# Kernel optimization log

Hardware: AMD Instinct MI355X
Metric: run time of the kernel (lower is better)

The kernel has to match this reference:

```python
import jax, jax.numpy as jnp
import numpy as np

B, S, H, E, K = 8, 4096, 1024, 256, 64
NEG = -1e30  # finite stand-in for -inf to keep grads NaN-free


def setup_inputs() -> dict:
    key = jax.random.key(0)
    ks = jax.random.split(key, 8)
    Hq = H // 4
    sc = 0.02
    return {
        "hidden_states": jax.random.normal(ks[0], (B, S, H), dtype=jnp.float32),
        "attention_mask": jnp.ones((B, S), dtype=jnp.int32),
        "block_boundaries": jnp.sort(jax.random.randint(ks[1], (B, K), 0, S), axis=-1),
        "tok_w1": jax.random.normal(ks[2], (H, Hq), dtype=jnp.float32) * sc,
        "tok_b1": jnp.zeros((Hq,), dtype=jnp.float32),
        "tok_w2": jax.random.normal(ks[3], (Hq, 1), dtype=jnp.float32) * sc,
        "tok_b2": jnp.zeros((1,), dtype=jnp.float32),
        "blk_w1": jax.random.normal(ks[4], (H, Hq), dtype=jnp.float32) * sc,
        "blk_b1": jnp.zeros((Hq,), dtype=jnp.float32),
        "blk_w2": jax.random.normal(ks[5], (Hq, 1), dtype=jnp.float32) * sc,
        "blk_b2": jnp.zeros((1,), dtype=jnp.float32),
        "out_w": jax.random.normal(ks[6], (H, E), dtype=jnp.float32) * sc,
        "out_b": jnp.zeros((E,), dtype=jnp.float32),
    }


def _attn_scores(x, w1, b1, w2, b2):
    # Linear -> Tanh -> Linear(.,1), squeeze last dim
    return (jnp.tanh(x @ w1 + b1) @ w2 + b2)[..., 0]


def reference(hidden_states, attention_mask, block_boundaries,
              tok_w1, tok_b1, tok_w2, tok_b2,
              blk_w1, blk_b1, blk_w2, blk_b2,
              out_w, out_b):
    Bz, Sz, Hz = hidden_states.shape
    Kz = block_boundaries.shape[1]
    pos = jnp.arange(Sz)
    # token -> block id: last boundary <= pos (tokens before first boundary get -1)
    block_id = jax.vmap(lambda bnd: jnp.searchsorted(bnd, pos, side='right') - 1)(block_boundaries)  # [B,S]
    member = block_id[:, :, None] == jnp.arange(Kz)[None, None, :]      # [B,S,K]
    valid = (attention_mask == 1) & (block_id >= 0)                     # [B,S]
    m_full = member & valid[:, :, None]                                 # [B,S,K]

    # stage 1: per-block masked softmax over tokens
    tok_scores = _attn_scores(hidden_states, tok_w1, tok_b1, tok_w2, tok_b2)  # [B,S]
    s = jnp.where(m_full, tok_scores[:, :, None], NEG)
    mx = jnp.max(s, axis=1, keepdims=True)                              # [B,1,K]
    e = jnp.where(m_full, jnp.exp(tok_scores[:, :, None] - mx), 0.0)
    denom = jnp.sum(e, axis=1, keepdims=True)                           # [B,1,K]
    w = jnp.where(denom > 0, e / jnp.maximum(denom, 1e-30), 0.0)
    block_embed = jnp.einsum('bsk,bsd->bkd', w, hidden_states)          # [B,K,H]
    block_valid = denom[:, 0, :] > 0                                    # [B,K] (empty blocks dropped)

    # stage 2: softmax over (non-empty) blocks
    blk_scores = _attn_scores(block_embed, blk_w1, blk_b1, blk_w2, blk_b2)    # [B,K]
    blk_scores = jnp.where(block_valid, blk_scores, NEG)
    bw = jax.nn.softmax(blk_scores, axis=-1)
    func = jnp.einsum('bk,bkd->bd', bw, block_embed)                    # [B,H]

    out = func @ out_w + out_b                                          # [B,E]
    return out / jnp.maximum(jnp.linalg.norm(out, axis=-1, keepdims=True), 1e-12)
```

## Files before the change

kernel.cpp:

```cpp
#include <hip/hip_runtime.h>
#include <math.h>
#include <limits.h>

#define BB 8
#define SS 4096
#define HH 1024
#define EE 256
#define KK 64
#define HQ 256
#define NEGF -1e30f

typedef short bf16x8 __attribute__((ext_vector_type(8)));
typedef float f32x4  __attribute__((ext_vector_type(4)));

__device__ inline short f2bf(float x) {
    unsigned u = __float_as_uint(x);
    unsigned r = (u + 0x7fffu + ((u >> 16) & 1u)) >> 16;
    return (short)r;
}

__device__ inline unsigned pk2bf(float lo, float hi) {
    unsigned a = __float_as_uint(lo) + 0x8000u;
    unsigned b = __float_as_uint(hi) + 0x8000u;
    return (a >> 16) | (b & 0xffff0000u);
}

__global__ __launch_bounds__(256) void convert_both_kernel(
    const float* __restrict__ tok_w1, const float* __restrict__ blk_w1,
    short* __restrict__ w1s_tok, short* __restrict__ w1s_blk)
{
    const int kb = blockIdx.x & 31, which = blockIdx.x >> 5;
    const float* src = which ? blk_w1 : tok_w1;
    short* dst = which ? w1s_blk : w1s_tok;
    const int n = threadIdx.x;
    for (int kk = 0; kk < 32; kk++)
        dst[kb * 8192 + n * 32 + kk] = f2bf(src[(kb * 32 + kk) * HQ + n]);
}

__global__ __launch_bounds__(256, 4) void mfma_score4_kernel(
    const float* __restrict__ X, const short* __restrict__ w1s,
    const float* __restrict__ b1, const float* __restrict__ w2,
    const float* __restrict__ b2, float* __restrict__ out)
{
    __shared__ __attribute__((aligned(16))) short As[2][1024];
    __shared__ float part[4][32];

    const int t = threadIdx.x;
    const int wv = t >> 6, lane = t & 63, lo = lane & 15, q = lane >> 4;
    const long row0 = (long)blockIdx.x * 32;

    f32x4 acc[2][4];
#pragma unroll
    for (int i = 0; i < 2; i++)
#pragma unroll
        for (int j = 0; j < 4; j++) acc[i][j] = (f32x4){0.f, 0.f, 0.f, 0.f};

    const int c = t >> 1, half = t & 1;
    const int srow = ((c >> 6) << 4) + (c & 15);
    const int skofs = ((c >> 4) & 3) * 8 + half * 4;
    const float* xs = X + (row0 + srow) * HH + skofs;
    short* const dst0 = &As[0][c * 8 + half * 4];
    short* const dst1 = &As[1][c * 8 + half * 4];
    const short* wp = w1s + (wv * 64 + lo) * 32 + q * 8;

    {
        float4 v = *(const float4*)xs;
        unsigned u0 = pk2bf(v.x, v.y), u1 = pk2bf(v.z, v.w);
        ((unsigned*)dst0)[0] = u0; ((unsigned*)dst0)[1] = u1;
    }
    bf16x8 bA[4], bB[4];
#pragma unroll
    for (int ct = 0; ct < 4; ct++)
        bA[ct] = *(const bf16x8*)(wp + ct * 512);
    __syncthreads();

    for (int kb = 0; kb < 32; kb += 2) {
        {
            float4 v = *(const float4*)(xs + (kb + 1) * 32);
#pragma unroll
            for (int ct = 0; ct < 4; ct++)
                bB[ct] = *(const bf16x8*)(wp + (kb + 1) * 8192 + ct * 512);
            bf16x8 af[2];
#pragma unroll
            for (int rt = 0; rt < 2; rt++)
                af[rt] = *(bf16x8*)(&As[0][(rt * 64 + q * 16 + lo) * 8]);
#pragma unroll
            for (int rt = 0; rt < 2; rt++)
#pragma unroll
                for (int ct = 0; ct < 4; ct++)
                    acc[rt][ct] = __builtin_amdgcn_mfma_f32_16x16x32_bf16(
                        af[rt], bA[ct], acc[rt][ct], 0, 0, 0);
            unsigned u0 = pk2bf(v.x, v.y), u1 = pk2bf(v.z, v.w);
            ((unsigned*)dst1)[0] = u0; ((unsigned*)dst1)[1] = u1;
        }
        __syncthreads();
        {
            const int k2 = (kb + 2 < 32) ? kb + 2 : 31;
            float4 v = *(const float4*)(xs + k2 * 32);
#pragma unroll
            for (int ct = 0; ct < 4; ct++)
                bA[ct] = *(const bf16x8*)(wp + k2 * 8192 + ct * 512);
            bf16x8 af[2];
#pragma unroll
            for (int rt = 0; rt < 2; rt++)
                af[rt] = *(bf16x8*)(&As[1][(rt * 64 + q * 16 + lo) * 8]);
#pragma unroll
            for (int rt = 0; rt < 2; rt++)
#pragma unroll
                for (int ct = 0; ct < 4; ct++)
                    acc[rt][ct] = __builtin_amdgcn_mfma_f32_16x16x32_bf16(
                        af[rt], bB[ct], acc[rt][ct], 0, 0, 0);
            unsigned u0 = pk2bf(v.x, v.y), u1 = pk2bf(v.z, v.w);
            ((unsigned*)dst0)[0] = u0; ((unsigned*)dst0)[1] = u1;
        }
        __syncthreads();
    }

    float rowpart[2][4];
#pragma unroll
    for (int rt = 0; rt < 2; rt++)
#pragma unroll
        for (int r = 0; r < 4; r++) rowpart[rt][r] = 0.f;
#pragma unroll
    for (int ct = 0; ct < 4; ct++) {
        const int cc = wv * 64 + ct * 16 + lo;
        const float b1c = b1[cc], w2c = w2[cc];
#pragma unroll
        for (int rt = 0; rt < 2; rt++)
#pragma unroll
            for (int r = 0; r < 4; r++)
                rowpart[rt][r] += tanhf(acc[rt][ct][r] + b1c) * w2c;
    }
#pragma unroll
    for (int rt = 0; rt < 2; rt++)
#pragma unroll
        for (int r = 0; r < 4; r++) {
            float v = rowpart[rt][r];
            v += __shfl_down(v, 8, 64);
            v += __shfl_down(v, 4, 64);
            v += __shfl_down(v, 2, 64);
            v += __shfl_down(v, 1, 64);
            rowpart[rt][r] = v;
        }
    if (lo == 0)
#pragma unroll
        for (int rt = 0; rt < 2; rt++)
#pragma unroll
            for (int r = 0; r < 4; r++)
                part[wv][rt * 16 + q * 4 + r] = rowpart[rt][r];
    __syncthreads();
    if (t < 32)
        out[row0 + t] = part[0][t] + part[1][t] + part[2][t] + part[3][t] + b2[0];
}

__global__ __launch_bounds__(256) void block_stats_kernel(
    const float* __restrict__ scores, const int* __restrict__ mask,
    const int* __restrict__ bnd, float* __restrict__ bden,
    float* __restrict__ wtok, float* __restrict__ embed)
{
    const int b = blockIdx.x >> 6, k = blockIdx.x & 63;
    const int start = bnd[b * KK + k];
    const int end = (k == KK - 1) ? SS : bnd[b * KK + k + 1];
    const int tid = threadIdx.x;
    __shared__ float r[4];
    __shared__ float mshared, dshared;

    *((float4*)(embed + (long)blockIdx.x * HH) + tid) = (float4){0.f, 0.f, 0.f, 0.f};
    if (k == 0)
        for (int s = tid; s < start; s += 256) wtok[b * SS + s] = 0.f;

    float m = NEGF;
    for (int s = start + tid; s < end; s += 256)
        if (mask[b * SS + s] == 1) m = fmaxf(m, scores[b * SS + s]);
    for (int off = 32; off > 0; off >>= 1) m = fmaxf(m, __shfl_down(m, off, 64));
    if ((tid & 63) == 0) r[tid >> 6] = m;
    __syncthreads();
    if (tid == 0) mshared = fmaxf(fmaxf(r[0], r[1]), fmaxf(r[2], r[3]));
    __syncthreads();
    m = mshared;

    float d = 0.f;
    for (int s = start + tid; s < end; s += 256)
        if (mask[b * SS + s] == 1) d += expf(scores[b * SS + s] - m);
    for (int off = 32; off > 0; off >>= 1) d += __shfl_down(d, off, 64);
    __syncthreads();
    if ((tid & 63) == 0) r[tid >> 6] = d;
    __syncthreads();
    if (tid == 0) {
        float den = r[0] + r[1] + r[2] + r[3];
        bden[blockIdx.x] = den;
        dshared = (den > 0.f) ? 1.f / fmaxf(den, 1e-30f) : 0.f;
    }
    __syncthreads();
    const float inv = dshared;
    for (int s = start + tid; s < end; s += 256)
        wtok[b * SS + s] = (mask[b * SS + s] == 1) ? expf(scores[b * SS + s] - m) * inv : 0.f;
}

#define TCH 16
__global__ __launch_bounds__(256) void block_embed4_kernel(
    const float* __restrict__ hidden, const float* __restrict__ wtok,
    const int* __restrict__ bnd, float* __restrict__ embed)
{
    const int b = blockIdx.x >> 8;
    const int ch = blockIdx.x & 255;
    const int t = threadIdx.x;
    __shared__ int bsh[KK];
    __shared__ float wsh[TCH];
    const int s0 = ch * TCH, s1 = s0 + TCH;
    if (t < KK) bsh[t] = bnd[b * KK + t];
    if (t >= 64 && t < 64 + TCH) wsh[t - 64] = wtok[b * SS + s0 + (t - 64)];
    __syncthreads();

    int cur = -1;
#pragma unroll
    for (int i = 0; i < KK; i++) cur = (bsh[i] <= s0) ? i : cur;
    const int nxt = (cur + 1 < KK) ? bsh[cur + 1] : INT_MAX;

    const float* hr0 = hidden + ((long)b * SS + s0) * HH + t;
    float a0 = 0.f, a1 = 0.f, a2 = 0.f, a3 = 0.f;

    if (nxt >= s1 && cur >= 0) {
#pragma unroll
        for (int i = 0; i < TCH; i++) {
            const float w = wsh[i];
            const float* hr = hr0 + (long)i * HH;
            a0 = fmaf(w, hr[0], a0);
            a1 = fmaf(w, hr[256], a1);
            a2 = fmaf(w, hr[512], a2);
            a3 = fmaf(w, hr[768], a3);
        }
        float* e = embed + ((long)b * KK + cur) * HH;
        atomicAdd(e + t, a0); atomicAdd(e + t + 256, a1);
        atomicAdd(e + t + 512, a2); atomicAdd(e + t + 768, a3);
        return;
    }

    bool any = false;
    for (int s = s0; s < s1; s++) {
        while (cur + 1 < KK && bsh[cur + 1] <= s) {
            if (any) {
                float* e = embed + ((long)b * KK + cur) * HH;
                atomicAdd(e + t, a0); atomicAdd(e + t + 256, a1);
                atomicAdd(e + t + 512, a2); atomicAdd(e + t + 768, a3);
                a0 = a1 = a2 = a3 = 0.f; any = false;
            }
            cur++;
        }
        if (cur < 0) continue;
        const float w = wsh[s - s0];
        const float* hr = hr0 + (long)(s - s0) * HH;
        a0 = fmaf(w, hr[0], a0);
        a1 = fmaf(w, hr[256], a1);
        a2 = fmaf(w, hr[512], a2);
        a3 = fmaf(w, hr[768], a3);
        any = true;
    }
    if (any) {
        float* e = embed + ((long)b * KK + cur) * HH;
        atomicAdd(e + t, a0); atomicAdd(e + t + 256, a1);
        atomicAdd(e + t + 512, a2); atomicAdd(e + t + 768, a3);
    }
}

__global__ __launch_bounds__(256) void finalize_ab_kernel(
    const float* __restrict__ embed, const float* __restrict__ bscores,
    const float* __restrict__ bden, const float* __restrict__ out_w,
    float* __restrict__ osum)
{
    const int b = blockIdx.x >> 3, hc = blockIdx.x & 7;
    const int t = threadIdx.x;
    __shared__ float bw[KK];
    __shared__ float fpart[2][128];
    __shared__ float fsh[128];

    if (t < KK) {
        float s = (bden[b * KK + t] > 0.f) ? bscores[b * KK + t] : NEGF;
        float m = s;
        for (int off = 32; off > 0; off >>= 1) m = fmaxf(m, __shfl_xor(m, off, 64));
        float e = expf(s - m);
        float d = e;
        for (int off = 32; off > 0; off >>= 1) d += __shfl_xor(d, off, 64);
        bw[t] = e / d;
    }
    __syncthreads();

    {
        const int hh = t & 127, kh = t >> 7;
        const float* ep = embed + ((long)b * KK + kh * 32) * HH + hc * 128 + hh;
        float f = 0.f;
#pragma unroll 8
        for (int k2 = 0; k2 < 32; k2++)
            f = fmaf(bw[kh * 32 + k2], ep[(long)k2 * HH], f);
        fpart[kh][hh] = f;
    }
    __syncthreads();
    if (t < 128) fsh[t] = fpart[0][t] + fpart[1][t];
    __syncthreads();

    float acc = 0.f;
    const float* wpp = out_w + (long)(hc * 128) * EE + t;
#pragma unroll 8
    for (int h = 0; h < 128; h++)
        acc = fmaf(fsh[h], wpp[(long)h * EE], acc);
    osum[(long)(b * 8 + hc) * EE + t] = acc;
}

__global__ __launch_bounds__(256) void finalize_c_kernel(
    const float* __restrict__ osum, const float* __restrict__ out_b,
    float* __restrict__ outp)
{
    const int b = blockIdx.x, t = threadIdx.x;
    __shared__ float r4[4];
    float o = out_b[t];
#pragma unroll
    for (int hc = 0; hc < 8; hc++)
        o += osum[(long)(b * 8 + hc) * EE + t];
    float sq = o * o;
    for (int off = 32; off > 0; off >>= 1) sq += __shfl_down(sq, off, 64);
    if ((t & 63) == 0) r4[t >> 6] = sq;
    __syncthreads();
    const float nrm = sqrtf(r4[0] + r4[1] + r4[2] + r4[3]);
    outp[b * EE + t] = o / fmaxf(nrm, 1e-12f);
}

extern "C" void kernel_launch(void* const* d_in, const int* in_sizes, int n_in,
                              void* d_out, int out_size, void* d_ws, size_t ws_size,
                              hipStream_t stream) {
    const float* hidden  = (const float*)d_in[0];
    const int*   mask    = (const int*)  d_in[1];
    const int*   bnd     = (const int*)  d_in[2];
    const float* tok_w1  = (const float*)d_in[3];
    const float* tok_b1  = (const float*)d_in[4];
    const float* tok_w2  = (const float*)d_in[5];
    const float* tok_b2  = (const float*)d_in[6];
    const float* blk_w1  = (const float*)d_in[7];
    const float* blk_b1  = (const float*)d_in[8];
    const float* blk_w2  = (const float*)d_in[9];
    const float* blk_b2  = (const float*)d_in[10];
    const float* out_w   = (const float*)d_in[11];
    const float* out_b   = (const float*)d_in[12];

    float* ws      = (float*)d_ws;
    float* wtok    = ws;
    float* embed   = ws + 32768;
    float* scores  = ws + 557056;
    float* bden    = ws + 589824;
    float* bscores = ws + 590336;
    float* osum    = ws + 590848;
    short* w1s_tok = (short*)(ws + 607232);
    short* w1s_blk = w1s_tok + 262144;

    convert_both_kernel<<<64, 256, 0, stream>>>(tok_w1, blk_w1, w1s_tok, w1s_blk);
    mfma_score4_kernel<<<BB * SS / 32, 256, 0, stream>>>(
        hidden, w1s_tok, tok_b1, tok_w2, tok_b2, scores);
    block_stats_kernel<<<BB * KK, 256, 0, stream>>>(
        scores, mask, bnd, bden, wtok, embed);
    block_embed4_kernel<<<BB * SS / TCH, 256, 0, stream>>>(hidden, wtok, bnd, embed);
    mfma_score4_kernel<<<BB * KK / 32, 256, 0, stream>>>(
        embed, w1s_blk, blk_b1, blk_w2, blk_b2, bscores);
    finalize_ab_kernel<<<BB * 8, 256, 0, stream>>>(
        embed, bscores, bden, out_w, osum);
    finalize_c_kernel<<<BB, 256, 0, stream>>>(osum, out_b, (float*)d_out);
}
```

Before: 300.7 us.

## Stage full 32-row activation tile in padded LDS and drop per-step barriers

Measured after the change: 312.2 us. +3.8%, slower.

```diff
diff --git a/kernel.cpp b/kernel.cpp
--- a/kernel.cpp
+++ b/kernel.cpp
@@ -37,83 +37,75 @@
         dst[kb * 8192 + n * 32 + kk] = f2bf(src[(kb * 32 + kk) * HQ + n]);
 }
 
-__global__ __launch_bounds__(256, 4) void mfma_score4_kernel(
+#define APAD 1032
+__global__ __launch_bounds__(256) void mfma_score5_kernel(
     const float* __restrict__ X, const short* __restrict__ w1s,
     const float* __restrict__ b1, const float* __restrict__ w2,
     const float* __restrict__ b2, float* __restrict__ out)
 {
-    __shared__ __attribute__((aligned(16))) short As[2][1024];
+    __shared__ __attribute__((aligned(16))) short As[32 * APAD];
     __shared__ float part[4][32];
 
     const int t = threadIdx.x;
     const int wv = t >> 6, lane = t & 63, lo = lane & 15, q = lane >> 4;
     const long row0 = (long)blockIdx.x * 32;
 
+    const float* xbase = X + row0 * HH + wv * 256 + lane * 4;
+#pragma unroll 8
+    for (int i = 0; i < 32; i++) {
+        float4 v = *(const float4*)(xbase + (long)i * HH);
+        unsigned u0 = pk2bf(v.x, v.y), u1 = pk2bf(v.z, v.w);
+        uint2* d = (uint2*)(&As[i * APAD + wv * 256 + lane * 4]);
+        *d = (uint2){u0, u1};
+    }
+    __syncthreads();
+
     f32x4 acc[2][4];
 #pragma unroll
     for (int i = 0; i < 2; i++)
 #pragma unroll
         for (int j = 0; j < 4; j++) acc[i][j] = (f32x4){0.f, 0.f, 0.f, 0.f};
 
-    const int c = t >> 1, half = t & 1;
-    const int srow = ((c >> 6) << 4) + (c & 15);
-    const int skofs = ((c >> 4) & 3) * 8 + half * 4;
-    const float* xs = X + (row0 + srow) * HH + skofs;
-    short* const dst0 = &As[0][c * 8 + half * 4];
-    short* const dst1 = &As[1][c * 8 + half * 4];
     const short* wp = w1s + (wv * 64 + lo) * 32 + q * 8;
-
-    {
-        float4 v = *(const float4*)xs;
-        unsigned u0 = pk2bf(v.x, v.y), u1 = pk2bf(v.z, v.w);
-        ((unsigned*)dst0)[0] = u0; ((unsigned*)dst0)[1] = u1;
-    }
+    const int aofs = lo * APAD + q * 8;
+
     bf16x8 bA[4], bB[4];
 #pragma unroll
     for (int ct = 0; ct < 4; ct++)
         bA[ct] = *(const bf16x8*)(wp + ct * 512);
-    __syncthreads();
 
     for (int kb = 0; kb < 32; kb += 2) {
         {
-            float4 v = *(const float4*)(xs + (kb + 1) * 32);
 #pragma unroll
             for (int ct = 0; ct < 4; ct++)
                 bB[ct] = *(const bf16x8*)(wp + (kb + 1) * 8192 + ct * 512);
             bf16x8 af[2];
 #pragma unroll
             for (int rt = 0; rt < 2; rt++)
-                af[rt] = *(bf16x8*)(&As[0][(rt * 64 + q * 16 + lo) * 8]);
+                af[rt] = *(bf16x8*)(&As[aofs + rt * 16 * APAD + kb * 32]);
 #pragma unroll
             for (int rt = 0; rt < 2; rt++)
 #pragma unroll
                 for (int ct = 0; ct < 4; ct++)
                     acc[rt][ct] = __builtin_amdgcn_mfma_f32_16x16x32_bf16(
                         af[rt], bA[ct], acc[rt][ct], 0, 0, 0);
-            unsigned u0 = pk2bf(v.x, v.y), u1 = pk2bf(v.z, v.w);
-            ((unsigned*)dst1)[0] = u0; ((unsigned*)dst1)[1] = u1;
-        }
-        __syncthreads();
+        }
         {
             const int k2 = (kb + 2 < 32) ? kb + 2 : 31;
-            float4 v = *(const float4*)(xs + k2 * 32);
 #pragma unroll
             for (int ct = 0; ct < 4; ct++)
                 bA[ct] = *(const bf16x8*)(wp + k2 * 8192 + ct * 512);
             bf16x8 af[2];
 #pragma unroll
             for (int rt = 0; rt < 2; rt++)
-                af[rt] = *(bf16x8*)(&As[1][(rt * 64 + q * 16 + lo) * 8]);
+                af[rt] = *(bf16x8*)(&As[aofs + rt * 16 * APAD + (kb + 1) * 32]);
 #pragma unroll
             for (int rt = 0; rt < 2; rt++)
 #pragma unroll
                 for (int ct = 0; ct < 4; ct++)
                     acc[rt][ct] = __builtin_amdgcn_mfma_f32_16x16x32_bf16(
                         af[rt], bB[ct], acc[rt][ct], 0, 0, 0);
-            unsigned u0 = pk2bf(v.x, v.y), u1 = pk2bf(v.z, v.w);
-            ((unsigned*)dst0)[0] = u0; ((unsigned*)dst0)[1] = u1;
-        }
-        __syncthreads();
+        }
     }
 
     float rowpart[2][4];
@@ -352,12 +344,12 @@
     short* w1s_blk = w1s_tok + 262144;
 
     convert_both_kernel<<<64, 256, 0, stream>>>(tok_w1, blk_w1, w1s_tok, w1s_blk);
-    mfma_score4_kernel<<<BB * SS / 32, 256, 0, stream>>>(
+    mfma_score5_kernel<<<BB * SS / 32, 256, 0, stream>>>(
         hidden, w1s_tok, tok_b1, tok_w2, tok_b2, scores);
     block_stats_kernel<<<BB * KK, 256, 0, stream>>>(
         scores, mask, bnd, bden, wtok, embed);
     block_embed4_kernel<<<BB * SS / TCH, 256, 0, stream>>>(hidden, wtok, bnd, embed);
-    mfma_score4_kernel<<<BB * KK / 32, 256, 0, stream>>>(
+    mfma_score5_kernel<<<BB * KK / 32, 256, 0, stream>>>(
         embed, w1s_blk, blk_b1, blk_w2, blk_b2, bscores);
     finalize_ab_kernel<<<BB * 8, 256, 0, stream>>>(
         embed, bscores, bden, out_w, osum);
```
